# Kernel optimization log

Hardware: AMD Instinct MI355X
Metric: run time of the kernel (lower is better)

The kernel has to match this reference:

```python
import jax, jax.numpy as jnp
import numpy as np
from jax import lax

E = 30      # embedding_dim
NH = 3      # attention heads
HD = E // NH
EPS = 1e-5


def _layer_norm(x, g, b):
    mu = jnp.mean(x, axis=-1, keepdims=True)
    var = jnp.mean(jnp.square(x - mu), axis=-1, keepdims=True)
    return (x - mu) * lax.rsqrt(var + EPS) * g + b


def setup_inputs() -> dict:
    key = jax.random.key(0)
    ks = jax.random.split(key, 16)
    B, T = 4096, 512
    s = 0.1  # param init scale
    return {
        "input": jax.random.normal(ks[0], (B, T, 5), jnp.float32),
        "w_ih": jax.random.normal(ks[1], (4 * E, 5), jnp.float32) * s,
        "w_hh": jax.random.normal(ks[2], (4 * E, E), jnp.float32) * s,
        "b_ih": jax.random.normal(ks[3], (4 * E,), jnp.float32) * s,
        "b_hh": jax.random.normal(ks[4], (4 * E,), jnp.float32) * s,
        "in_proj_w": jax.random.normal(ks[5], (3 * E, E), jnp.float32) * s,
        "in_proj_b": jax.random.normal(ks[6], (3 * E,), jnp.float32) * s,
        "out_proj_w": jax.random.normal(ks[7], (E, E), jnp.float32) * s,
        "out_proj_b": jax.random.normal(ks[8], (E,), jnp.float32) * s,
        "fc1_w": jax.random.normal(ks[9], (E, E), jnp.float32) * s,
        "fc1_b": jax.random.normal(ks[10], (E,), jnp.float32) * s,
        "fc2_w": jax.random.normal(ks[11], (E, E), jnp.float32) * s,
        "fc2_b": jax.random.normal(ks[12], (E,), jnp.float32) * s,
        "ln_g": jnp.ones((E,), jnp.float32),
        "ln_b": jnp.zeros((E,), jnp.float32),
        "out_w": jax.random.normal(ks[13], (3, E), jnp.float32) * s,
        "out_b": jax.random.normal(ks[14], (3,), jnp.float32) * s,
    }


def reference(input, w_ih, w_hh, b_ih, b_hh, in_proj_w, in_proj_b,
              out_proj_w, out_proj_b, fc1_w, fc1_b, fc2_w, fc2_b,
              ln_g, ln_b, out_w, out_b):
    B = input.shape[0]
    # --- LSTM (1 layer, batch_first); gate order i,f,g,o as in torch ---
    x_proj = jnp.einsum('bti,gi->btg', input, w_ih) + b_ih + b_hh  # [B,T,4E]

    def step(carry, xg):
        h, c = carry
        gates = xg + h @ w_hh.T
        i, f, g, o = jnp.split(gates, 4, axis=-1)
        i = jax.nn.sigmoid(i); f = jax.nn.sigmoid(f)
        g = jnp.tanh(g); o = jax.nn.sigmoid(o)
        c = f * c + i * g
        h = o * jnp.tanh(c)
        return (h, c), None

    h0 = jnp.zeros((B, E), input.dtype)
    (h_n, c_n), _ = lax.scan(step, (h0, h0), x_proj.transpose(1, 0, 2))

    # --- MultiheadAttention on 2D inputs: torch treats [B,E] as unbatched
    # sequences of length B, so attention mixes across the batch axis. ---
    q = h_n @ in_proj_w[:E].T + in_proj_b[:E]
    k = c_n @ in_proj_w[E:2 * E].T + in_proj_b[E:2 * E]
    v = c_n @ in_proj_w[2 * E:].T + in_proj_b[2 * E:]
    qh = q.reshape(B, NH, HD).transpose(1, 0, 2)  # [NH, B, HD]
    kh = k.reshape(B, NH, HD).transpose(1, 0, 2)
    vh = v.reshape(B, NH, HD).transpose(1, 0, 2)
    scores = jnp.einsum('hld,hmd->hlm', qh, kh) / np.sqrt(HD)  # [NH,B,B]
    attn = jax.nn.softmax(scores, axis=-1)
    ctx = jnp.einsum('hlm,hmd->hld', attn, vh)  # [NH,B,HD]
    attn_out = ctx.transpose(1, 0, 2).reshape(B, E) @ out_proj_w.T + out_proj_b

    # --- residual + shared LayerNorm + MLP (exact GELU) ---
    x1 = _layer_norm(attn_out + h_n, ln_g, ln_b)
    fc = jax.nn.gelu(x1 @ fc1_w.T + fc1_b, approximate=False) @ fc2_w.T + fc2_b
    x2 = _layer_norm(x1 + fc, ln_g, ln_b)
    return x2 @ out_w.T + out_b  # [B, 3]
```

## Files before the change

kernel.cpp:

```cpp
#include <hip/hip_runtime.h>
#include <math.h>

#define Bsz  4096
#define Tlen 512
#define NE   30
#define NIN  5
#define HD10 10
#define B10  (Bsz*HD10)

typedef _Float16 h2v  __attribute__((ext_vector_type(2)));
typedef _Float16 f16x8 __attribute__((ext_vector_type(8)));
typedef float    f32x4 __attribute__((ext_vector_type(4)));

__device__ __forceinline__ float fexp2(float x){ return __builtin_amdgcn_exp2f(x); }
__device__ __forceinline__ float frcp (float x){ return __builtin_amdgcn_rcpf(x); }
#define L2E 1.4426950408889634f

__device__ __forceinline__ void loadarr32(float arr[32], const float* bufrow){
  const float4* p4 = (const float4*)bufrow;
  #pragma unroll
  for (int q4=0;q4<8;q4++){ float4 vv=p4[q4]; arr[4*q4]=vv.x; arr[4*q4+1]=vv.y; arr[4*q4+2]=vv.z; arr[4*q4+3]=vv.w; }
}

#define XSTR 520

extern "C" __global__ void __launch_bounds__(512,1)
lstm_k(const float* __restrict__ input, const float* __restrict__ w_ih,
       const float* __restrict__ w_hh, const float* __restrict__ b_ih,
       const float* __restrict__ b_hh, const float* __restrict__ in_proj_w,
       const float* __restrict__ in_proj_b,
       float* __restrict__ qo, float* __restrict__ ko, float* __restrict__ vo,
       float* __restrict__ ho)
{
  __shared__ __align__(16) _Float16 hb[2*640];
  __shared__ __align__(16) _Float16 xh[16*XSTR];
  const int tid  = threadIdx.x;
  const int wv   = __builtin_amdgcn_readfirstlane(tid >> 6);
  const int lane = tid & 63;
  const int n    = lane & 15;
  const int quad = lane >> 4;
  const int b0   = blockIdx.x * 16;

  f16x8 ah[4], ax[4];
  f32x4 bi[4];
  #pragma unroll
  for (int G=0; G<4; ++G){
    const float sG = (G==2) ? (-2.f*L2E) : (-L2E);
    const int dA = 8*(n>>2) + ((wv + (n&3)) & 7);
    const bool rv = (dA < NE);
    const int grow = rv ? (NE*G + dA) : 0;
    #pragma unroll
    for (int j=0;j<8;++j){
      const int k = quad*8 + j;
      ah[G][j] = (rv && k < NE) ? (_Float16)(sG*w_hh[grow*NE + k]) : (_Float16)0;
      ax[G][j] = (rv && quad==0 && j < NIN) ? (_Float16)(sG*w_ih[grow*NIN + j]) : (_Float16)0;
    }
    #pragma unroll
    for (int r=0;r<4;++r){
      const int d = 8*quad + ((wv + r) & 7);
      bi[G][r] = (d < NE) ? sG*(b_ih[NE*G+d] + b_hh[NE*G+d]) : 0.f;
    }
  }
  for (int i=tid; i<640; i+=512) ((float*)hb)[i] = 0.f;
  for (int i=tid; i<16*XSTR; i+=512) xh[i] = (_Float16)0;
  __syncthreads();

  float cc=0.f, hh=0.f;
  const int rdo  = n*40 + 8*quad;
  const int wro  = n*40 + 8*quad + wv;
  const int xoff = n*XSTR;
  f16x8 xB;
  f32x4 Cx[4], Cy[4];

#define LSTM_STEP(CIN, COUT, RB, WB, TT2) do{ \
    const f16x8 bh_ = *(const f16x8*)(hb + (RB) + rdo); \
    _Pragma("unroll") \
    for (int G=0;G<4;++G) \
      COUT[G] = __builtin_amdgcn_mfma_f32_16x16x32_f16(ax[G], xB, bi[G], 0,0,0); \
    xB = *(const f16x8*)(xh + xoff + ((TT2)&63)*8); \
    f32x4 C_[4]; \
    _Pragma("unroll") \
    for (int G=0;G<4;++G) \
      C_[G] = __builtin_amdgcn_mfma_f32_16x16x32_f16(ah[G], bh_, CIN[G], 0,0,0); \
     \
    const float ei=fexp2(C_[0][0]), ef=fexp2(C_[1][0]); \
    const float eg=fexp2(C_[2][0]), eo=fexp2(C_[3][0]); \
    const float Af=1.f+ef, Bi_=1.f+ei, G2=1.f+eg; \
    cc = cc*frcp(Af) + (2.f-G2)*frcp(Bi_*G2); \
    const float e2=fexp2((2.f*L2E)*cc); \
    const float E2=1.f+e2; \
    hh = (E2-2.f)*frcp((1.f+eo)*E2); \
    hb[(WB) + wro] = (_Float16)hh; \
    __syncthreads(); \
  }while(0)

  for (int tc = 0; tc < Tlen; tc += 64) {
    for (int i4 = tid; i4 < 1280; i4 += 512){
      const int nn = i4/80, e4 = i4%80;
      const float4 v4 = *(const float4*)(input + (size_t)(b0+nn)*(Tlen*NIN) + tc*NIN + e4*4);
      #pragma unroll
      for (int u=0;u<4;++u){
        const int e = e4*4+u;
        xh[nn*XSTR + (e/5)*8 + (e%5)] = (_Float16)((&v4.x)[u]);
      }
    }
    __syncthreads();
    {
      const f16x8 x0 = *(const f16x8*)(xh + xoff);
      #pragma unroll
      for (int G=0;G<4;++G)
        Cx[G] = __builtin_amdgcn_mfma_f32_16x16x32_f16(ax[G], x0, bi[G], 0,0,0);
      xB = *(const f16x8*)(xh + xoff + 8);
    }
    #pragma unroll 1
    for (int tl = 0; tl < 64; tl += 2) {
      LSTM_STEP(Cx, Cy, 0,   640, tl+2);
      LSTM_STEP(Cy, Cx, 640, 0,   tl+3);
    }
  }
#undef LSTM_STEP

  float* hf = (float*)xh;
  float* cf = hf + 16*36;
  {
    hf[n*36 + 8*quad + wv] = hh;
    cf[n*36 + 8*quad + wv] = cc;
  }
  __syncthreads();
  for (int i = tid; i < 16*NE; i += 512){
    const int nn = i/NE, d = i%NE;
    ho[(size_t)(b0+nn)*NE + d] = hf[nn*36 + d];
  }
  const float QS = 0.31622776601683794f;
  for (int i = tid; i < 90*16; i += 512){
    const int o  = i % 90;
    const int nn = i / 90;
    const float* wrow = in_proj_w + o*NE;
    const float* src  = (o < NE) ? &hf[nn*36] : &cf[nn*36];
    float acc = in_proj_b[o];
    #pragma unroll
    for (int k2=0;k2<NE;k2++) acc = fmaf(wrow[k2], src[k2], acc);
    const int b = b0 + nn;
    if (o < 30)      { qo[(o/10)*B10 + b*10 + (o%10)] = acc * QS; }
    else if (o < 60) { const int u=o-30; ko[(u/10)*B10 + b*10 + (u%10)] = acc; }
    else             { const int u=o-60; vo[(u/10)*B10 + b*10 + (u%10)] = acc; }
  }
}

extern "C" __global__ void __launch_bounds__(256)
attn_part(const float* __restrict__ q, const float* __restrict__ k,
          const float* __restrict__ v, float* __restrict__ part, int nkeys)
{
  __shared__ __align__(16) float kst[640];
  __shared__ __align__(16) float vst[640];
  const int t    = threadIdx.x;
  const int qr   = blockIdx.x*256 + t;
  const int head = blockIdx.y;
  const int ks   = blockIdx.z;
  const float* kh = k + (size_t)head*B10;
  const float* vh = v + (size_t)head*B10;
  float qreg[10];
  {
    const float2* qp = (const float2*)(q + (size_t)head*B10 + (size_t)qr*10);
    #pragma unroll
    for (int i=0;i<5;i++){ float2 t2=qp[i]; qreg[2*i]=t2.x; qreg[2*i+1]=t2.y; }
  }
  float m = -INFINITY, l = 0.f, acc[10];
  #pragma unroll
  for (int d=0;d<10;d++) acc[d]=0.f;

  const int k0 = ks * nkeys;
  const int nt = nkeys >> 6;
  #pragma unroll 1
  for (int ti=0; ti<nt; ++ti){
    const int kt0 = k0 + (ti<<6);
    __syncthreads();
    {
      const float4* ksrc = (const float4*)(kh + (size_t)kt0*10);
      const float4* vsrc = (const float4*)(vh + (size_t)kt0*10);
      for (int i=t; i<320; i+=256){
        if (i < 160) ((float4*)kst)[i]     = ksrc[i];
        else         ((float4*)vst)[i-160] = vsrc[i-160];
      }
    }
    __syncthreads();
    #pragma unroll 1
    for (int c8=0; c8<64; c8+=8){
      float s[8];
      #pragma unroll
      for (int u=0;u<8;u++){
        const float2* kp = (const float2*)(kst + (c8+u)*10);
        float sv = 0.f;
        #pragma unroll
        for (int i=0;i<5;i++){ float2 kk=kp[i]; sv=fmaf(qreg[2*i],kk.x,sv); sv=fmaf(qreg[2*i+1],kk.y,sv); }
        s[u]=sv;
      }
      float mc = s[0];
      #pragma unroll
      for (int u=1;u<8;u++) mc = fmaxf(mc, s[u]);
      const float mnew = fmaxf(m, mc);
      const float corr = fexp2(L2E*(m - mnew));
      l *= corr;
      #pragma unroll
      for (int d=0;d<10;d++) acc[d]*=corr;
      #pragma unroll
      for (int u=0;u<8;u++){
        const float p = fexp2(L2E*(s[u]-mnew));
        l += p;
        const float2* vp = (const float2*)(vst + (c8+u)*10);
        #pragma unroll
        for (int i=0;i<5;i++){ float2 vv=vp[i]; acc[2*i]=fmaf(p,vv.x,acc[2*i]); acc[2*i+1]=fmaf(p,vv.y,acc[2*i+1]); }
      }
      m = mnew;
    }
  }
  float* pp = part + ((size_t)(head*Bsz + qr)*gridDim.z + ks)*12;
  pp[0]=m; pp[1]=l;
  #pragma unroll
  for (int d=0;d<10;d++) pp[2+d]=acc[d];
}

extern "C" __global__ void __launch_bounds__(256)
tail_k(const float* __restrict__ part, int ns, const float* __restrict__ hn,
       const float* __restrict__ out_proj_w, const float* __restrict__ out_proj_b,
       const float* __restrict__ fc1_w, const float* __restrict__ fc1_b,
       const float* __restrict__ fc2_w, const float* __restrict__ fc2_b,
       const float* __restrict__ ln_g, const float* __restrict__ ln_b,
       const float* __restrict__ out_w, const float* __restrict__ out_b,
       float* __restrict__ out)
{
  __shared__ __align__(16) float buf[4][32];
  __shared__ float wl[2880];
  const int tidb = threadIdx.x;
  for (int i=tidb;i<900;i+=256) wl[i]       = out_proj_w[i];
  for (int i=tidb;i<900;i+=256) wl[900+i]   = fc1_w[i];
  for (int i=tidb;i<900;i+=256) wl[1800+i]  = fc2_w[i];
  if (tidb < 90) wl[2700+tidb] = out_w[tidb];
  const int wave = tidb >> 6;
  const int lane = tidb & 63;
  const int b = blockIdx.x*4 + wave;
  const bool act = (lane < NE);
  if (lane < 32) buf[wave][lane] = 0.f;
  __syncthreads();
  if (act) {
    const int head = lane/10, dd = lane%10;
    const float* p = part + ((size_t)(head*Bsz + b)*ns)*12;
    float M = -INFINITY, L = 0.f, O = 0.f;
    for (int i=0;i<ns;i++){
      const float mi = p[i*12], li = p[i*12+1], ai = p[i*12+2+dd];
      const float Mn = fmaxf(M, mi);
      const float cw = fexp2(L2E*(M - Mn));
      const float wi = fexp2(L2E*(mi - Mn));
      L = fmaf(li, wi, L*cw);
      O = fmaf(ai, wi, O*cw);
      M = Mn;
    }
    buf[wave][lane] = O / L;
  }
  __builtin_amdgcn_wave_barrier();
  float arr[32];
  loadarr32(arr, &buf[wave][0]);
  const float hv = act ? hn[b*NE+lane] : 0.f;
  float x = 0.f;
  if (act) {
    float a = out_proj_b[lane];
    #pragma unroll
    for (int k2=0;k2<NE;k2++) a = fmaf(wl[lane*NE+k2], arr[k2], a);
    x = a + hv;
  }
  __builtin_amdgcn_wave_barrier();
  if (act) buf[wave][lane] = x;
  __builtin_amdgcn_wave_barrier();
  loadarr32(arr, &buf[wave][0]);
  float s1=0.f, s2=0.f;
  #pragma unroll
  for (int k2=0;k2<32;k2++){ s1+=arr[k2]; s2=fmaf(arr[k2],arr[k2],s2); }
  float mu = s1*(1.f/30.f);
  float var = s2*(1.f/30.f) - mu*mu;
  float rs = rsqrtf(var + 1e-5f);
  float x1 = 0.f;
  if (act) x1 = fmaf((x-mu)*rs, ln_g[lane], ln_b[lane]);
  __builtin_amdgcn_wave_barrier();
  if (act) buf[wave][lane] = x1;
  __builtin_amdgcn_wave_barrier();
  loadarr32(arr, &buf[wave][0]);
  float gv = 0.f;
  if (act) {
    float a = fc1_b[lane];
    #pragma unroll
    for (int k2=0;k2<NE;k2++) a = fmaf(wl[900+lane*NE+k2], arr[k2], a);
    gv = 0.5f*a*(1.f + erff(a*0.70710678118654752f));
  }
  __builtin_amdgcn_wave_barrier();
  if (act) buf[wave][lane] = gv;
  __builtin_amdgcn_wave_barrier();
  loadarr32(arr, &buf[wave][0]);
  float y = 0.f;
  if (act) {
    float a = fc2_b[lane];
    #pragma unroll
    for (int k2=0;k2<NE;k2++) a = fmaf(wl[1800+lane*NE+k2], arr[k2], a);
    y = x1 + a;
  }
  __builtin_amdgcn_wave_barrier();
  if (act) buf[wave][lane] = y;
  __builtin_amdgcn_wave_barrier();
  loadarr32(arr, &buf[wave][0]);
  s1=0.f; s2=0.f;
  #pragma unroll
  for (int k2=0;k2<32;k2++){ s1+=arr[k2]; s2=fmaf(arr[k2],arr[k2],s2); }
  mu = s1*(1.f/30.f);
  var = s2*(1.f/30.f) - mu*mu;
  rs = rsqrtf(var + 1e-5f);
  float x2 = 0.f;
  if (act) x2 = fmaf((y-mu)*rs, ln_g[lane], ln_b[lane]);
  __builtin_amdgcn_wave_barrier();
  if (act) buf[wave][lane] = x2;
  __builtin_amdgcn_wave_barrier();
  loadarr32(arr, &buf[wave][0]);
  if (lane < 3) {
    float a = out_b[lane];
    #pragma unroll
    for (int k2=0;k2<NE;k2++) a = fmaf(wl[2700+lane*NE+k2], arr[k2], a);
    out[b*3 + lane] = a;
  }
}

extern "C" void kernel_launch(void* const* d_in, const int* in_sizes, int n_in,
                              void* d_out, int out_size, void* d_ws, size_t ws_size,
                              hipStream_t stream)
{
  const float* input      = (const float*)d_in[0];
  const float* w_ih       = (const float*)d_in[1];
  const float* w_hh       = (const float*)d_in[2];
  const float* b_ih       = (const float*)d_in[3];
  const float* b_hh       = (const float*)d_in[4];
  const float* in_proj_w  = (const float*)d_in[5];
  const float* in_proj_b  = (const float*)d_in[6];
  const float* out_proj_w = (const float*)d_in[7];
  const float* out_proj_b = (const float*)d_in[8];
  const float* fc1_w      = (const float*)d_in[9];
  const float* fc1_b      = (const float*)d_in[10];
  const float* fc2_w      = (const float*)d_in[11];
  const float* fc2_b      = (const float*)d_in[12];
  const float* ln_g       = (const float*)d_in[13];
  const float* ln_b       = (const float*)d_in[14];
  const float* out_w      = (const float*)d_in[15];
  const float* out_b      = (const float*)d_in[16];

  float* ws = (float*)d_ws;
  float* qo   = ws;
  float* ko   = ws + 122880;
  float* vo   = ws + 245760;
  float* hn   = ws + 368640;
  float* part = ws + 491520;

  const size_t need16 = ((size_t)491520 + (size_t)3*4096*16*12) * 4;
  const int NS = (ws_size >= need16) ? 16 : 8;

  lstm_k<<<Bsz/16, 512, 0, stream>>>(input, w_ih, w_hh, b_ih, b_hh,
                                     in_proj_w, in_proj_b, qo, ko, vo, hn);
  attn_part<<<dim3(Bsz/256, 3, NS), 256, 0, stream>>>(qo, ko, vo, part, Bsz/NS);
  tail_k<<<Bsz/4, 256, 0, stream>>>(part, NS, hn, out_proj_w, out_proj_b,
                                    fc1_w, fc1_b, fc2_w, fc2_b,
                                    ln_g, ln_b, out_w, out_b, (float*)d_out);
}
```

Baseline: 318.3 us.

## Interleave LSTM gate rows so one MFMA yields all four gates per lane

Reorders the recurrent and input weight rows in the MFMA A operand so that the four output rows of each lane's 16x16 accumulator tile hold the i, f, g, o gates for the same hidden unit. Each timestep then needs one recurrent MFMA and one input-projection MFMA instead of four of each. This shortens the serial per-step dependency chain and cuts matrix-core work and register use. The gate scaling and bias mapping are reworked to match the new row layout, which risks indexing mistakes.

After: 289.4 us. 9.1% less time.

```diff
diff --git a/kernel.cpp b/kernel.cpp
--- a/kernel.cpp
+++ b/kernel.cpp
@@ -41,24 +41,26 @@
   const int quad = lane >> 4;
   const int b0   = blockIdx.x * 16;
 
-  f16x8 ah[4], ax[4];
-  f32x4 bi[4];
-  #pragma unroll
-  for (int G=0; G<4; ++G){
-    const float sG = (G==2) ? (-2.f*L2E) : (-L2E);
-    const int dA = 8*(n>>2) + ((wv + (n&3)) & 7);
+  f16x8 ah, ax;
+  f32x4 bi;
+  {
+    const int r  = n & 3;
+    const int qm = n >> 2;
+    const int dA = 8*qm + wv;
+    const float sG = (r==2) ? (-2.f*L2E) : (-L2E);
     const bool rv = (dA < NE);
-    const int grow = rv ? (NE*G + dA) : 0;
+    const int grow = rv ? (r*NE + dA) : 0;
     #pragma unroll
     for (int j=0;j<8;++j){
       const int k = quad*8 + j;
-      ah[G][j] = (rv && k < NE) ? (_Float16)(sG*w_hh[grow*NE + k]) : (_Float16)0;
-      ax[G][j] = (rv && quad==0 && j < NIN) ? (_Float16)(sG*w_ih[grow*NIN + j]) : (_Float16)0;
-    }
-    #pragma unroll
-    for (int r=0;r<4;++r){
-      const int d = 8*quad + ((wv + r) & 7);
-      bi[G][r] = (d < NE) ? sG*(b_ih[NE*G+d] + b_hh[NE*G+d]) : 0.f;
+      ah[j] = (rv && k < NE) ? (_Float16)(sG*w_hh[grow*NE + k]) : (_Float16)0;
+      ax[j] = (rv && quad==0 && j < NIN) ? (_Float16)(sG*w_ih[grow*NIN + j]) : (_Float16)0;
+    }
+    const int d = 8*quad + wv;
+    #pragma unroll
+    for (int rr=0;rr<4;++rr){
+      const float sR = (rr==2) ? (-2.f*L2E) : (-L2E);
+      bi[rr] = (d < NE) ? sR*(b_ih[rr*NE+d] + b_hh[rr*NE+d]) : 0.f;
     }
   }
   for (int i=tid; i<640; i+=512) ((float*)hb)[i] = 0.f;
@@ -70,21 +72,16 @@
   const int wro  = n*40 + 8*quad + wv;
   const int xoff = n*XSTR;
   f16x8 xB;
-  f32x4 Cx[4], Cy[4];
+  f32x4 Cx, Cy;
 
 #define LSTM_STEP(CIN, COUT, RB, WB, TT2) do{ \
     const f16x8 bh_ = *(const f16x8*)(hb + (RB) + rdo); \
-    _Pragma("unroll") \
-    for (int G=0;G<4;++G) \
-      COUT[G] = __builtin_amdgcn_mfma_f32_16x16x32_f16(ax[G], xB, bi[G], 0,0,0); \
+    COUT = __builtin_amdgcn_mfma_f32_16x16x32_f16(ax, xB, bi, 0,0,0); \
     xB = *(const f16x8*)(xh + xoff + ((TT2)&63)*8); \
-    f32x4 C_[4]; \
-    _Pragma("unroll") \
-    for (int G=0;G<4;++G) \
-      C_[G] = __builtin_amdgcn_mfma_f32_16x16x32_f16(ah[G], bh_, CIN[G], 0,0,0); \
+    f32x4 C_ = __builtin_amdgcn_mfma_f32_16x16x32_f16(ah, bh_, CIN, 0,0,0); \
      \
-    const float ei=fexp2(C_[0][0]), ef=fexp2(C_[1][0]); \
-    const float eg=fexp2(C_[2][0]), eo=fexp2(C_[3][0]); \
+    const float ei=fexp2(C_[0]), ef=fexp2(C_[1]); \
+    const float eg=fexp2(C_[2]), eo=fexp2(C_[3]); \
     const float Af=1.f+ef, Bi_=1.f+ei, G2=1.f+eg; \
     cc = cc*frcp(Af) + (2.f-G2)*frcp(Bi_*G2); \
     const float e2=fexp2((2.f*L2E)*cc); \
@@ -107,9 +104,7 @@
     __syncthreads();
     {
       const f16x8 x0 = *(const f16x8*)(xh + xoff);
-      #pragma unroll
-      for (int G=0;G<4;++G)
-        Cx[G] = __builtin_amdgcn_mfma_f32_16x16x32_f16(ax[G], x0, bi[G], 0,0,0);
+      Cx = __builtin_amdgcn_mfma_f32_16x16x32_f16(ax, x0, bi, 0,0,0);
       xB = *(const f16x8*)(xh + xoff + 8);
     }
     #pragma unroll 1
```
